# Optimization experiments

Measured on AMD Instinct MI355X. Metric: run time of the kernel, lower is better.

The kernel has to match this reference:

```python
import jax, jax.numpy as jnp
import numpy as np

OUTPUT_SIZE = 512


def _build_schedule(n, m):
    """Static pyramid-circuit schedule of Givens/RBS gates on n wires.

    Sequential gate order (matches theta ordering): for k = 1..n-1, apply
    gates on adjacent wire pairs (i, i+1) for i = k-1 down to max(k-m, 0).
    Total gates = (2n - m - 1) * m // 2. Gates are packed into a brickwork
    schedule (timestep t = 2(k-1) - i) so each layer touches disjoint pairs
    and the whole chain runs in T = n + m - 2 parallel layers.
    Padded slots point at dummy wires (n, n+1) and are masked to identity.
    """
    layers = {}
    t_idx = 0
    for k in range(1, n):
        for i in range(k - 1, max(k - m, 0) - 1, -1):
            t = 2 * (k - 1) - i
            layers.setdefault(t, []).append((i, t_idx))
            t_idx += 1
    T = max(layers) + 1
    W = max(len(v) for v in layers.values())
    wire = np.full((T, W), n, dtype=np.int32)   # pad gates hit dummy wires (n, n+1)
    tidx = np.zeros((T, W), dtype=np.int32)
    mask = np.zeros((T, W), dtype=np.float32)
    for t, gs in layers.items():
        for j, (i, ti) in enumerate(gs):
            wire[t, j] = i
            tidx[t, j] = ti
            mask[t, j] = 1.0
    return wire, tidx, mask


def apply_orthogonal(thetas, x, output_size):
    input_size = x.shape[-1]
    n, m = max(input_size, output_size), min(input_size, output_size)
    wire, tidx, mask = _build_schedule(n, m)
    if input_size < n:
        x = jnp.pad(x, ((0, 0), (0, n - input_size)))
    state = jnp.pad(x, ((0, 0), (0, 2)))          # two dummy columns for padded gate slots
    th = thetas[jnp.asarray(tidx)]                # [T, W]
    msk = jnp.asarray(mask)
    cos = jnp.where(msk > 0, jnp.cos(th), 1.0)    # padded slots -> identity rotation
    sin = jnp.where(msk > 0, jnp.sin(th), 0.0)
    wa = jnp.asarray(wire)                        # [T, W] first wire of each pair
    wb = wa + 1

    def step(st, layer):
        c, s, a_idx, b_idx = layer
        a = st[:, a_idx]                          # [B, W]
        b = st[:, b_idx]
        st = st.at[:, a_idx].set(c * a + s * b)   # RBS rotation on each pair
        st = st.at[:, b_idx].set(c * b - s * a)
        return st, None

    state, _ = jax.lax.scan(step, state, (cos, sin, wa, wb))
    return state[:, :output_size]


def setup_inputs():
    key = jax.random.key(0)
    k1, k2 = jax.random.split(key)
    B, N = 256, 512
    n_thetas = (2 * max(N, OUTPUT_SIZE) - min(N, OUTPUT_SIZE) - 1) * min(N, OUTPUT_SIZE) // 2
    x = jax.random.normal(k1, (B, N), dtype=jnp.float32)
    thetas = jax.random.uniform(k2, (n_thetas,), dtype=jnp.float32,
                                minval=-np.pi, maxval=np.pi)
    bias = jnp.zeros((OUTPUT_SIZE,), dtype=jnp.float32)
    return {"x": x, "thetas": thetas, "bias": bias}


def reference(x, thetas, bias):
    # normalize_inputs=False path; with_bias=True
    out = apply_orthogonal(thetas, x, OUTPUT_SIZE)
    return out + bias
```

## Files before the change

kernel.cpp:

```cpp
#include <hip/hip_runtime.h>
#include <hip/hip_fp16.h>
#include <stdint.h>


#define PAIRS_PAD 512
#define TOTALH2 (PAIRS_PAD * 512)
#define NWIN 8
#define WPAIRS 64
#define V_ELEMS (512 * 512)

#define OFF_V_BYTES (1u << 20)
#define V_BYTES (512u * 512u * 2u)
#define OFF_P_BYTES (OFF_V_BYTES + 8u * V_BYTES)
#define OFF_Q_BYTES (OFF_P_BYTES + 4u * V_BYTES)
#define OFF_Y_BYTES (OFF_Q_BYTES + 2u * V_BYTES)

typedef _Float16 half8_t __attribute__((ext_vector_type(8)));
typedef float f32x4_t __attribute__((ext_vector_type(4)));

__global__ __launch_bounds__(256) void fused_kernel(
    const float* __restrict__ thetas, __half2* __restrict__ Wh) {
  int tid = blockIdx.x * 256 + threadIdx.x;
  int p = tid >> 9, r = tid & 511;
  int h = r >> 8, rr = r & 255, L = rr >> 2, j = rr & 3;
  int t = 2 * p + h;
  int i = 8 * L + 2 * j + h;
  float c = 1.0f, s = 0.0f;
  if (i <= min(t, 1020 - t)) {
    int k = ((t + i) >> 1) + 1;
    int idx = ((k * (k - 1)) >> 1) + (k - 1 - i);
    __sincosf(thetas[idx], &s, &c);
  }
  if (h == 1 && j == 3) c -= 1.0f;
  Wh[tid] = __floats2half2_rn(c, s);
}

template <int N>
__device__ __forceinline__ void wait_vm() {
  asm volatile("s_waitcnt vmcnt(%0)" ::"i"(N) : "memory");
}
template <int CTRL>
__device__ __forceinline__ float dpp_f(float v) {
  return __int_as_float(
      __builtin_amdgcn_mov_dpp(__float_as_int(v), CTRL, 0xF, 0xF, true));
}
template <int CTRL>
__device__ __forceinline__ uint32_t dpp_u(uint32_t v) {
  return (uint32_t)__builtin_amdgcn_mov_dpp((int)v, CTRL, 0xF, 0xF, true);
}
__device__ __forceinline__ float mix_s(uint32_t g, float b) {
  float d;
  asm("v_fma_mix_f32 %0, %1, %2, 0 op_sel:[1,0,0] op_sel_hi:[1,0,0]"
      : "=v"(d) : "v"(g), "v"(b));
  return d;
}
__device__ __forceinline__ float mix_ns(uint32_t g, float b) {
  float d;
  asm("v_fma_mix_f32 %0, -%1, %2, 0 op_sel:[1,0,0] op_sel_hi:[1,0,0]"
      : "=v"(d) : "v"(g), "v"(b));
  return d;
}
__device__ __forceinline__ float mix_c_acc(uint32_t g, float b, float acc) {
  float d;
  asm("v_fma_mix_f32 %0, %1, %2, %3 op_sel:[0,0,0] op_sel_hi:[1,0,0]"
      : "=v"(d) : "v"(g), "v"(b), "v"(acc));
  return d;
}
__device__ __forceinline__ void gate_mix(float& a, float& b, uint32_t g) {
  float t = mix_s(g, b);
  float u = mix_ns(g, a);
  float na = mix_c_acc(g, a, t);
  float nb = mix_c_acc(g, b, u);
  a = na; b = nb;
}
__device__ __forceinline__ void gate_mix_neg(float& a, float& b, uint32_t g) {
  float t = mix_ns(g, b);
  float u = mix_s(g, a);
  float na = mix_c_acc(g, a, t);
  float nb = mix_c_acc(g, b, u);
  a = na; b = nb;
}

__device__ __forceinline__ void pair_fwd(float& v0, float& v1, float& v2,
                                         float& v3, float& v4, float& v5,
                                         float& v6, float& v7,
                                         const uint4& E, const uint4& O) {
  gate_mix(v0, v1, E.x);
  gate_mix(v2, v3, E.y);
  gate_mix(v4, v5, E.z);
  gate_mix(v6, v7, E.w);
  uint32_t bl = dpp_u<0x111>(O.w);
  float rv0 = dpp_f<0x101>(v0);
  float lv7 = dpp_f<0x111>(v7);
  gate_mix(v1, v2, O.x);
  gate_mix(v3, v4, O.y);
  gate_mix(v5, v6, O.z);
  float t = mix_s(O.w, rv0);
  t = mix_c_acc(O.w, v7, t);
  v7 = t + v7;
  float u = mix_ns(bl, lv7);
  u = mix_c_acc(bl, v0, u);
  v0 = u + v0;
}

__device__ __forceinline__ void pair_rev(float& v0, float& v1, float& v2,
                                         float& v3, float& v4, float& v5,
                                         float& v6, float& v7,
                                         const uint4& E, const uint4& O) {
  uint32_t bl = dpp_u<0x111>(O.w);
  float rv0 = dpp_f<0x101>(v0);
  float lv7 = dpp_f<0x111>(v7);
  gate_mix_neg(v1, v2, O.x);
  gate_mix_neg(v3, v4, O.y);
  gate_mix_neg(v5, v6, O.z);
  float t = mix_ns(O.w, rv0);
  t = mix_c_acc(O.w, v7, t);
  v7 = t + v7;
  float u = mix_s(bl, lv7);
  u = mix_c_acc(bl, v0, u);
  v0 = u + v0;
  gate_mix_neg(v0, v1, E.x);
  gate_mix_neg(v2, v3, E.y);
  gate_mix_neg(v4, v5, E.z);
  gate_mix_neg(v6, v7, E.w);
}

__global__ __launch_bounds__(64) void window_kernel(
    const uint32_t* __restrict__ W, _Float16* __restrict__ V) {
  const int lane = threadIdx.x;
  const int gl = lane & 15, grp = lane >> 4;
  const int w = blockIdx.x >> 7;
  const int d = ((blockIdx.x & 127) << 2) + grp;
  const bool rev = (w & 1);
  int b0 = d - 60;
  int base = (b0 <= 0) ? 0 : (b0 & ~7);
  base = min(base, 384);
  const int idx0 = (base >> 3) + gl;
  const int wire0 = base + 8 * gl;

  float v0 = (wire0 + 0 == d) ? 1.f : 0.f;
  float v1 = (wire0 + 1 == d) ? 1.f : 0.f;
  float v2 = (wire0 + 2 == d) ? 1.f : 0.f;
  float v3 = (wire0 + 3 == d) ? 1.f : 0.f;
  float v4 = (wire0 + 4 == d) ? 1.f : 0.f;
  float v5 = (wire0 + 5 == d) ? 1.f : 0.f;
  float v6 = (wire0 + 6 == d) ? 1.f : 0.f;
  float v7 = (wire0 + 7 == d) ? 1.f : 0.f;

  const int p0 = w * WPAIRS;
  const uint4* __restrict__ Wg = (const uint4*)W;

  uint4 R[4][2];
  if (!rev) {
#pragma unroll
    for (int s = 0; s < 4; ++s) {
      R[s][0] = Wg[(p0 + s) * 128 + idx0];
      R[s][1] = Wg[(p0 + s) * 128 + 64 + idx0];
    }
    for (int it = 0; it < 16; ++it) {
#pragma unroll
      for (int s = 0; s < 4; ++s) {
        wait_vm<6>();
        pair_fwd(v0, v1, v2, v3, v4, v5, v6, v7, R[s][0], R[s][1]);
        int pn = p0 + min(it * 4 + s + 4, 63);
        R[s][0] = Wg[pn * 128 + idx0];
        R[s][1] = Wg[pn * 128 + 64 + idx0];
      }
    }
  } else {
#pragma unroll
    for (int s = 0; s < 4; ++s) {
      R[s][0] = Wg[(p0 + 63 - s) * 128 + idx0];
      R[s][1] = Wg[(p0 + 63 - s) * 128 + 64 + idx0];
    }
    for (int it = 0; it < 16; ++it) {
#pragma unroll
      for (int s = 0; s < 4; ++s) {
        wait_vm<6>();
        pair_rev(v0, v1, v2, v3, v4, v5, v6, v7, R[s][0], R[s][1]);
        int pn = p0 + 63 - min(it * 4 + s + 4, 63);
        R[s][0] = Wg[pn * 128 + idx0];
        R[s][1] = Wg[pn * 128 + 64 + idx0];
      }
    }
  }

  uint32_t ph0 = __builtin_bit_cast(uint32_t, __builtin_amdgcn_cvt_pkrtz(v0, v1));
  uint32_t ph1 = __builtin_bit_cast(uint32_t, __builtin_amdgcn_cvt_pkrtz(v2, v3));
  uint32_t ph2 = __builtin_bit_cast(uint32_t, __builtin_amdgcn_cvt_pkrtz(v4, v5));
  uint32_t ph3 = __builtin_bit_cast(uint32_t, __builtin_amdgcn_cvt_pkrtz(v6, v7));
  uint32_t* dst = (uint32_t*)(V + (size_t)w * V_ELEMS + (size_t)d * 512);
#pragma unroll
  for (int pass = 0; pass < 4; ++pass) {
    const int S = ((pass << 7) - base) >> 3;
    const int srcg = gl + S;
    const bool ok = (srcg >= 0) && (srcg < 16);
    const int baddr = ((grp << 4) + (ok ? srcg : 0)) << 2;
    uint32_t o0 = (uint32_t)__builtin_amdgcn_ds_bpermute(baddr, (int)ph0);
    uint32_t o1 = (uint32_t)__builtin_amdgcn_ds_bpermute(baddr, (int)ph1);
    uint32_t o2 = (uint32_t)__builtin_amdgcn_ds_bpermute(baddr, (int)ph2);
    uint32_t o3 = (uint32_t)__builtin_amdgcn_ds_bpermute(baddr, (int)ph3);
    if (!ok) { o0 = 0u; o1 = 0u; o2 = 0u; o3 = 0u; }
    *(uint4*)(dst + pass * 64 + gl * 4) = make_uint4(o0, o1, o2, o3);
  }
}

struct GemmDesc { const _Float16* A; const _Float16* B; _Float16* C; };
struct Descs4 { GemmDesc d[4]; };

__global__ __launch_bounds__(128) void gemm512_kernel(Descs4 ds) {
  const int g = blockIdx.x >> 7;
  const int t = blockIdx.x & 127;
  const int rt = t >> 3, ct = t & 7;
  const int lane = threadIdx.x & 63, wv = threadIdx.x >> 6;
  const int l16 = lane & 15, h8 = (lane >> 4) * 8;
  const GemmDesc de = ds.d[g];
  const _Float16* Ap = de.A + (size_t)(rt * 32 + wv * 16 + l16) * 512 + h8;
  const _Float16* Bp = de.B + (size_t)(ct * 64 + l16) * 512 + h8;

  half8_t aR[3]; half8_t bR[3][4];
#pragma unroll
  for (int s = 0; s < 3; ++s) {
    aR[s] = *(const half8_t*)(Ap + s * 32);
#pragma unroll
    for (int n = 0; n < 4; ++n)
      bR[s][n] = *(const half8_t*)(Bp + (size_t)n * (16 * 512) + s * 32);
  }
  f32x4_t acc[4];
#pragma unroll
  for (int n = 0; n < 4; ++n) acc[n] = (f32x4_t){0.f, 0.f, 0.f, 0.f};

#pragma unroll
  for (int ks = 0; ks < 16; ++ks) {
    const int s = ks % 3;
    if (ks <= 13) wait_vm<10>();
    else if (ks == 14) wait_vm<5>();
    else wait_vm<0>();
    half8_t a = aR[s];
    half8_t b0 = bR[s][0], b1 = bR[s][1], b2 = bR[s][2], b3 = bR[s][3];
    if (ks + 3 < 16) {
      aR[s] = *(const half8_t*)(Ap + (ks + 3) * 32);
#pragma unroll
      for (int n = 0; n < 4; ++n)
        bR[s][n] = *(const half8_t*)(Bp + (size_t)n * (16 * 512) + (ks + 3) * 32);
    }
    acc[0] = __builtin_amdgcn_mfma_f32_16x16x32_f16(a, b0, acc[0], 0, 0, 0);
    acc[1] = __builtin_amdgcn_mfma_f32_16x16x32_f16(a, b1, acc[1], 0, 0, 0);
    acc[2] = __builtin_amdgcn_mfma_f32_16x16x32_f16(a, b2, acc[2], 0, 0, 0);
    acc[3] = __builtin_amdgcn_mfma_f32_16x16x32_f16(a, b3, acc[3], 0, 0, 0);
  }
  const int r4 = rt * 32 + wv * 16 + (lane >> 4) * 4;
#pragma unroll
  for (int n = 0; n < 4; ++n) {
    uint2 pk;
    pk.x = __builtin_bit_cast(uint32_t,
             __builtin_amdgcn_cvt_pkrtz(acc[n][0], acc[n][1]));
    pk.y = __builtin_bit_cast(uint32_t,
             __builtin_amdgcn_cvt_pkrtz(acc[n][2], acc[n][3]));
    *(uint2*)(de.C + (size_t)(ct * 64 + n * 16 + l16) * 512 + r4) = pk;
  }
}

__global__ __launch_bounds__(128) void apply1_kernel(
    const _Float16* __restrict__ Qt0, const float* __restrict__ x,
    _Float16* __restrict__ y) {
  const int rt = blockIdx.x >> 2, ct = blockIdx.x & 3;
  const int lane = threadIdx.x & 63, wv = threadIdx.x >> 6;
  const int l16 = lane & 15, h8 = (lane >> 4) * 8;
  const _Float16* Ap = Qt0 + (size_t)(rt * 32 + wv * 16 + l16) * 512 + h8;
  const float* Bx = x + (size_t)(ct * 64 + l16) * 512 + h8;

  half8_t aR[2]; float4 fR[2][4][2];
#pragma unroll
  for (int s = 0; s < 2; ++s) {
    aR[s] = *(const half8_t*)(Ap + s * 32);
#pragma unroll
    for (int n = 0; n < 4; ++n) {
      fR[s][n][0] = *(const float4*)(Bx + (size_t)n * (16 * 512) + s * 32);
      fR[s][n][1] = *(const float4*)(Bx + (size_t)n * (16 * 512) + s * 32 + 4);
    }
  }
  f32x4_t acc[4];
#pragma unroll
  for (int n = 0; n < 4; ++n) acc[n] = (f32x4_t){0.f, 0.f, 0.f, 0.f};

#pragma unroll
  for (int ks = 0; ks < 16; ++ks) {
    const int s = ks & 1;
    if (ks <= 14) wait_vm<9>();
    else wait_vm<0>();
    half8_t a = aR[s];
    half8_t bf[4];
#pragma unroll
    for (int n = 0; n < 4; ++n) {
      float4 f0 = fR[s][n][0], f1 = fR[s][n][1];
      uint4 u;
      u.x = __builtin_bit_cast(uint32_t, __builtin_amdgcn_cvt_pkrtz(f0.x, f0.y));
      u.y = __builtin_bit_cast(uint32_t, __builtin_amdgcn_cvt_pkrtz(f0.z, f0.w));
      u.z = __builtin_bit_cast(uint32_t, __builtin_amdgcn_cvt_pkrtz(f1.x, f1.y));
      u.w = __builtin_bit_cast(uint32_t, __builtin_amdgcn_cvt_pkrtz(f1.z, f1.w));
      bf[n] = __builtin_bit_cast(half8_t, u);
    }
    if (ks + 2 < 16) {
      aR[s] = *(const half8_t*)(Ap + (ks + 2) * 32);
#pragma unroll
      for (int n = 0; n < 4; ++n) {
        fR[s][n][0] = *(const float4*)(Bx + (size_t)n * (16 * 512) + (ks + 2) * 32);
        fR[s][n][1] = *(const float4*)(Bx + (size_t)n * (16 * 512) + (ks + 2) * 32 + 4);
      }
    }
    acc[0] = __builtin_amdgcn_mfma_f32_16x16x32_f16(a, bf[0], acc[0], 0, 0, 0);
    acc[1] = __builtin_amdgcn_mfma_f32_16x16x32_f16(a, bf[1], acc[1], 0, 0, 0);
    acc[2] = __builtin_amdgcn_mfma_f32_16x16x32_f16(a, bf[2], acc[2], 0, 0, 0);
    acc[3] = __builtin_amdgcn_mfma_f32_16x16x32_f16(a, bf[3], acc[3], 0, 0, 0);
  }
  const int r4 = rt * 32 + wv * 16 + (lane >> 4) * 4;
#pragma unroll
  for (int n = 0; n < 4; ++n) {
    uint2 pk;
    pk.x = __builtin_bit_cast(uint32_t,
             __builtin_amdgcn_cvt_pkrtz(acc[n][0], acc[n][1]));
    pk.y = __builtin_bit_cast(uint32_t,
             __builtin_amdgcn_cvt_pkrtz(acc[n][2], acc[n][3]));
    *(uint2*)(y + (size_t)(ct * 64 + n * 16 + l16) * 512 + r4) = pk;
  }
}

__global__ __launch_bounds__(128) void apply2_kernel(
    const _Float16* __restrict__ Qt1, const _Float16* __restrict__ y,
    const float* __restrict__ bias, float* __restrict__ out) {
  const int rt = blockIdx.x >> 2, ct = blockIdx.x & 3;
  const int lane = threadIdx.x & 63, wv = threadIdx.x >> 6;
  const int l16 = lane & 15, h8 = (lane >> 4) * 8;
  const _Float16* Ap = Qt1 + (size_t)(rt * 32 + wv * 16 + l16) * 512 + h8;
  const _Float16* Bp = y + (size_t)(ct * 64 + l16) * 512 + h8;

  half8_t aR[3]; half8_t bR[3][4];
#pragma unroll
  for (int s = 0; s < 3; ++s) {
    aR[s] = *(const half8_t*)(Ap + s * 32);
#pragma unroll
    for (int n = 0; n < 4; ++n)
      bR[s][n] = *(const half8_t*)(Bp + (size_t)n * (16 * 512) + s * 32);
  }
  f32x4_t acc[4];
#pragma unroll
  for (int n = 0; n < 4; ++n) acc[n] = (f32x4_t){0.f, 0.f, 0.f, 0.f};

#pragma unroll
  for (int ks = 0; ks < 16; ++ks) {
    const int s = ks % 3;
    if (ks <= 13) wait_vm<10>();
    else if (ks == 14) wait_vm<5>();
    else wait_vm<0>();
    half8_t a = aR[s];
    half8_t b0 = bR[s][0], b1 = bR[s][1], b2 = bR[s][2], b3 = bR[s][3];
    if (ks + 3 < 16) {
      aR[s] = *(const half8_t*)(Ap + (ks + 3) * 32);
#pragma unroll
      for (int n = 0; n < 4; ++n)
        bR[s][n] = *(const half8_t*)(Bp + (size_t)n * (16 * 512) + (ks + 3) * 32);
    }
    acc[0] = __builtin_amdgcn_mfma_f32_16x16x32_f16(a, b0, acc[0], 0, 0, 0);
    acc[1] = __builtin_amdgcn_mfma_f32_16x16x32_f16(a, b1, acc[1], 0, 0, 0);
    acc[2] = __builtin_amdgcn_mfma_f32_16x16x32_f16(a, b2, acc[2], 0, 0, 0);
    acc[3] = __builtin_amdgcn_mfma_f32_16x16x32_f16(a, b3, acc[3], 0, 0, 0);
  }
  const int r4 = rt * 32 + wv * 16 + (lane >> 4) * 4;
  const float4 bv = *(const float4*)(bias + r4);
#pragma unroll
  for (int n = 0; n < 4; ++n) {
    const int b = ct * 64 + n * 16 + l16;
    float4 o;
    o.x = acc[n][0] + bv.x;
    o.y = acc[n][1] + bv.y;
    o.z = acc[n][2] + bv.z;
    o.w = acc[n][3] + bv.w;
    *(float4*)(out + (size_t)b * 512 + r4) = o;
  }
}

extern "C" void kernel_launch(void* const* d_in, const int* in_sizes, int n_in,
                              void* d_out, int out_size, void* d_ws,
                              size_t ws_size, hipStream_t stream) {
  const float* x = (const float*)d_in[0];
  const float* thetas = (const float*)d_in[1];
  const float* bias = (const float*)d_in[2];
  float* out = (float*)d_out;

  char* ws = (char*)d_ws;
  uint32_t* W = (uint32_t*)ws;
  _Float16* V = (_Float16*)(ws + OFF_V_BYTES);
  _Float16* P = (_Float16*)(ws + OFF_P_BYTES);
  _Float16* Q = (_Float16*)(ws + OFF_Q_BYTES);
  _Float16* Y = (_Float16*)(ws + OFF_Y_BYTES);

  fused_kernel<<<TOTALH2 / 256, 256, 0, stream>>>(thetas, (__half2*)W);
  window_kernel<<<NWIN * 128, 64, 0, stream>>>(W, V);

  Descs4 l1;
  l1.d[0] = {V + 1 * (size_t)V_ELEMS, V + 0 * (size_t)V_ELEMS, P + 0 * (size_t)V_ELEMS};
  l1.d[1] = {V + 2 * (size_t)V_ELEMS, V + 3 * (size_t)V_ELEMS, P + 1 * (size_t)V_ELEMS};
  l1.d[2] = {V + 5 * (size_t)V_ELEMS, V + 4 * (size_t)V_ELEMS, P + 2 * (size_t)V_ELEMS};
  l1.d[3] = {V + 6 * (size_t)V_ELEMS, V + 7 * (size_t)V_ELEMS, P + 3 * (size_t)V_ELEMS};
  gemm512_kernel<<<512, 128, 0, stream>>>(l1);

  Descs4 l2;
  l2.d[0] = {P + 0 * (size_t)V_ELEMS, P + 1 * (size_t)V_ELEMS, Q + 0 * (size_t)V_ELEMS};
  l2.d[1] = {P + 2 * (size_t)V_ELEMS, P + 3 * (size_t)V_ELEMS, Q + 1 * (size_t)V_ELEMS};
  l2.d[2] = l2.d[0];
  l2.d[3] = l2.d[0];
  gemm512_kernel<<<256, 128, 0, stream>>>(l2);

  apply1_kernel<<<64, 128, 0, stream>>>(Q + 0 * (size_t)V_ELEMS, x, Y);
  apply2_kernel<<<64, 128, 0, stream>>>(Q + 1 * (size_t)V_ELEMS, Y, bias, out);
}
```

Baseline: 107.1 us.

## Fuse all stages into one cooperative persistent kernel with grid syncs

```diff
diff --git a/kernel.cpp b/kernel.cpp
--- a/kernel.cpp
+++ b/kernel.cpp
@@ -1,6 +1,9 @@
 #include <hip/hip_runtime.h>
 #include <hip/hip_fp16.h>
+#include <hip/hip_cooperative_groups.h>
 #include <stdint.h>
+
+namespace cg = cooperative_groups;
 
 
 #define PAIRS_PAD 512
@@ -17,23 +20,6 @@
 
 typedef _Float16 half8_t __attribute__((ext_vector_type(8)));
 typedef float f32x4_t __attribute__((ext_vector_type(4)));
-
-__global__ __launch_bounds__(256) void fused_kernel(
-    const float* __restrict__ thetas, __half2* __restrict__ Wh) {
-  int tid = blockIdx.x * 256 + threadIdx.x;
-  int p = tid >> 9, r = tid & 511;
-  int h = r >> 8, rr = r & 255, L = rr >> 2, j = rr & 3;
-  int t = 2 * p + h;
-  int i = 8 * L + 2 * j + h;
-  float c = 1.0f, s = 0.0f;
-  if (i <= min(t, 1020 - t)) {
-    int k = ((t + i) >> 1) + 1;
-    int idx = ((k * (k - 1)) >> 1) + (k - 1 - i);
-    __sincosf(thetas[idx], &s, &c);
-  }
-  if (h == 1 && j == 3) c -= 1.0f;
-  Wh[tid] = __floats2half2_rn(c, s);
-}
 
 template <int N>
 __device__ __forceinline__ void wait_vm() {
@@ -125,12 +111,30 @@
   gate_mix_neg(v6, v7, E.w);
 }
 
-__global__ __launch_bounds__(64) void window_kernel(
-    const uint32_t* __restrict__ W, _Float16* __restrict__ V) {
-  const int lane = threadIdx.x;
+
+__device__ __forceinline__ void dev_table(int tid,
+                                          const float* __restrict__ thetas,
+                                          __half2* __restrict__ Wh) {
+  int p = tid >> 9, r = tid & 511;
+  int h = r >> 8, rr = r & 255, L = rr >> 2, j = rr & 3;
+  int t = 2 * p + h;
+  int i = 8 * L + 2 * j + h;
+  float c = 1.0f, s = 0.0f;
+  if (i <= min(t, 1020 - t)) {
+    int k = ((t + i) >> 1) + 1;
+    int idx = ((k * (k - 1)) >> 1) + (k - 1 - i);
+    __sincosf(thetas[idx], &s, &c);
+  }
+  if (h == 1 && j == 3) c -= 1.0f;
+  Wh[tid] = __floats2half2_rn(c, s);
+}
+
+__device__ __forceinline__ void dev_window(int gw, int lane,
+                                           const uint32_t* __restrict__ W,
+                                           _Float16* __restrict__ V) {
   const int gl = lane & 15, grp = lane >> 4;
-  const int w = blockIdx.x >> 7;
-  const int d = ((blockIdx.x & 127) << 2) + grp;
+  const int w = gw >> 7;
+  const int d = ((gw & 127) << 2) + grp;
   const bool rev = (w & 1);
   int b0 = d - 60;
   int base = (b0 <= 0) ? 0 : (b0 & ~7);
@@ -205,18 +209,15 @@
   }
 }
 
-struct GemmDesc { const _Float16* A; const _Float16* B; _Float16* C; };
-struct Descs4 { GemmDesc d[4]; };
-
-__global__ __launch_bounds__(128) void gemm512_kernel(Descs4 ds) {
-  const int g = blockIdx.x >> 7;
-  const int t = blockIdx.x & 127;
+__device__ __forceinline__ void dev_gemm_tile(const _Float16* __restrict__ A,
+                                              const _Float16* __restrict__ B,
+                                              _Float16* __restrict__ C, int t,
+                                              int ut) {
   const int rt = t >> 3, ct = t & 7;
-  const int lane = threadIdx.x & 63, wv = threadIdx.x >> 6;
+  const int lane = ut & 63, wv = ut >> 6;
   const int l16 = lane & 15, h8 = (lane >> 4) * 8;
-  const GemmDesc de = ds.d[g];
-  const _Float16* Ap = de.A + (size_t)(rt * 32 + wv * 16 + l16) * 512 + h8;
-  const _Float16* Bp = de.B + (size_t)(ct * 64 + l16) * 512 + h8;
+  const _Float16* Ap = A + (size_t)(rt * 32 + wv * 16 + l16) * 512 + h8;
+  const _Float16* Bp = B + (size_t)(ct * 64 + l16) * 512 + h8;
 
   half8_t aR[3]; half8_t bR[3][4];
 #pragma unroll
@@ -257,15 +258,16 @@
              __builtin_amdgcn_cvt_pkrtz(acc[n][0], acc[n][1]));
     pk.y = __builtin_bit_cast(uint32_t,
              __builtin_amdgcn_cvt_pkrtz(acc[n][2], acc[n][3]));
-    *(uint2*)(de.C + (size_t)(ct * 64 + n * 16 + l16) * 512 + r4) = pk;
-  }
-}
-
-__global__ __launch_bounds__(128) void apply1_kernel(
-    const _Float16* __restrict__ Qt0, const float* __restrict__ x,
-    _Float16* __restrict__ y) {
-  const int rt = blockIdx.x >> 2, ct = blockIdx.x & 3;
-  const int lane = threadIdx.x & 63, wv = threadIdx.x >> 6;
+    *(uint2*)(C + (size_t)(ct * 64 + n * 16 + l16) * 512 + r4) = pk;
+  }
+}
+
+__device__ __forceinline__ void dev_apply1(int job, int ut,
+                                           const _Float16* __restrict__ Qt0,
+                                           const float* __restrict__ x,
+                                           _Float16* __restrict__ y) {
+  const int rt = job >> 2, ct = job & 3;
+  const int lane = ut & 63, wv = ut >> 6;
   const int l16 = lane & 15, h8 = (lane >> 4) * 8;
   const _Float16* Ap = Qt0 + (size_t)(rt * 32 + wv * 16 + l16) * 512 + h8;
   const float* Bx = x + (size_t)(ct * 64 + l16) * 512 + h8;
@@ -326,11 +328,13 @@
   }
 }
 
-__global__ __launch_bounds__(128) void apply2_kernel(
-    const _Float16* __restrict__ Qt1, const _Float16* __restrict__ y,
-    const float* __restrict__ bias, float* __restrict__ out) {
-  const int rt = blockIdx.x >> 2, ct = blockIdx.x & 3;
-  const int lane = threadIdx.x & 63, wv = threadIdx.x >> 6;
+__device__ __forceinline__ void dev_apply2(int job, int ut,
+                                           const _Float16* __restrict__ Qt1,
+                                           const _Float16* __restrict__ y,
+                                           const float* __restrict__ bias,
+                                           float* __restrict__ out) {
+  const int rt = job >> 2, ct = job & 3;
+  const int lane = ut & 63, wv = ut >> 6;
   const int l16 = lane & 15, h8 = (lane >> 4) * 8;
   const _Float16* Ap = Qt1 + (size_t)(rt * 32 + wv * 16 + l16) * 512 + h8;
   const _Float16* Bp = y + (size_t)(ct * 64 + l16) * 512 + h8;
@@ -380,11 +384,90 @@
   }
 }
 
+__global__ __launch_bounds__(256, 1) void mega_kernel(
+    const float* __restrict__ thetas, const float* __restrict__ x,
+    const float* __restrict__ bias, uint32_t* __restrict__ W,
+    _Float16* __restrict__ V, _Float16* __restrict__ P,
+    _Float16* __restrict__ Q, _Float16* __restrict__ Y,
+    float* __restrict__ out) {
+  cg::grid_group grid = cg::this_grid();
+  const int tid = threadIdx.x;
+  const int bid = blockIdx.x;
+  const int gtid = bid * 256 + tid;
+
+  {
+    __half2* Wh = (__half2*)W;
+#pragma unroll
+    for (int kk = 0; kk < 4; ++kk) dev_table(gtid + kk * 65536, thetas, Wh);
+  }
+  wait_vm<0>();
+  grid.sync();
+
+  dev_window(bid * 4 + (tid >> 6), tid & 63, W, V);
+  wait_vm<0>();
+  grid.sync();
+
+  const int unit = bid * 2 + (tid >> 7);
+  const int ut = tid & 127;
+
+  {
+    const int g = unit >> 7, t = unit & 127;
+    const int ag = g + 1 + ((g >> 1) << 1);
+    const int bg = 4 * g + 1 - ag;
+    dev_gemm_tile(V + (size_t)ag * V_ELEMS, V + (size_t)bg * V_ELEMS,
+                  P + (size_t)g * V_ELEMS, t, ut);
+  }
+  wait_vm<0>();
+  grid.sync();
+
+  if (unit < 256) {
+    const int g = unit >> 7, t = unit & 127;
+    dev_gemm_tile(P + (size_t)(2 * g) * V_ELEMS,
+                  P + (size_t)(2 * g + 1) * V_ELEMS,
+                  Q + (size_t)g * V_ELEMS, t, ut);
+    wait_vm<0>();
+  }
+  grid.sync();
+
+  if (unit < 64) {
+    dev_apply1(unit, ut, Q, x, Y);
+    wait_vm<0>();
+  }
+  grid.sync();
+
+  if (unit < 64) dev_apply2(unit, ut, Q + (size_t)V_ELEMS, Y, bias, out);
+}
+
+__global__ __launch_bounds__(256) void fused_kernel(
+    const float* __restrict__ thetas, __half2* __restrict__ Wh) {
+  dev_table(blockIdx.x * 256 + threadIdx.x, thetas, Wh);
+}
+__global__ __launch_bounds__(64) void window_kernel(
+    const uint32_t* __restrict__ W, _Float16* __restrict__ V) {
+  dev_window(blockIdx.x, threadIdx.x, W, V);
+}
+struct GemmDesc { const _Float16* A; const _Float16* B; _Float16* C; };
+struct Descs4 { GemmDesc d[4]; };
+__global__ __launch_bounds__(128) void gemm512_kernel(Descs4 ds) {
+  const GemmDesc de = ds.d[blockIdx.x >> 7];
+  dev_gemm_tile(de.A, de.B, de.C, blockIdx.x & 127, threadIdx.x);
+}
+__global__ __launch_bounds__(128) void apply1_kernel(
+    const _Float16* __restrict__ Qt0, const float* __restrict__ x,
+    _Float16* __restrict__ y) {
+  dev_apply1(blockIdx.x, threadIdx.x, Qt0, x, y);
+}
+__global__ __launch_bounds__(128) void apply2_kernel(
+    const _Float16* __restrict__ Qt1, const _Float16* __restrict__ y,
+    const float* __restrict__ bias, float* __restrict__ out) {
+  dev_apply2(blockIdx.x, threadIdx.x, Qt1, y, bias, out);
+}
+
 extern "C" void kernel_launch(void* const* d_in, const int* in_sizes, int n_in,
                               void* d_out, int out_size, void* d_ws,
                               size_t ws_size, hipStream_t stream) {
+  const float* thetas = (const float*)d_in[1];
   const float* x = (const float*)d_in[0];
-  const float* thetas = (const float*)d_in[1];
   const float* bias = (const float*)d_in[2];
   float* out = (float*)d_out;
 
@@ -395,23 +478,27 @@
   _Float16* Q = (_Float16*)(ws + OFF_Q_BYTES);
   _Float16* Y = (_Float16*)(ws + OFF_Y_BYTES);
 
+  void* args[] = {(void*)&thetas, (void*)&x, (void*)&bias, (void*)&W,
+                  (void*)&V, (void*)&P, (void*)&Q, (void*)&Y, (void*)&out};
+  hipError_t err = hipLaunchCooperativeKernel(
+      (void*)mega_kernel, dim3(256), dim3(256), args, 0, stream);
+  if (err == hipSuccess) return;
+  (void)hipGetLastError();
+
   fused_kernel<<<TOTALH2 / 256, 256, 0, stream>>>(thetas, (__half2*)W);
   window_kernel<<<NWIN * 128, 64, 0, stream>>>(W, V);
-
   Descs4 l1;
   l1.d[0] = {V + 1 * (size_t)V_ELEMS, V + 0 * (size_t)V_ELEMS, P + 0 * (size_t)V_ELEMS};
   l1.d[1] = {V + 2 * (size_t)V_ELEMS, V + 3 * (size_t)V_ELEMS, P + 1 * (size_t)V_ELEMS};
   l1.d[2] = {V + 5 * (size_t)V_ELEMS, V + 4 * (size_t)V_ELEMS, P + 2 * (size_t)V_ELEMS};
   l1.d[3] = {V + 6 * (size_t)V_ELEMS, V + 7 * (size_t)V_ELEMS, P + 3 * (size_t)V_ELEMS};
   gemm512_kernel<<<512, 128, 0, stream>>>(l1);
-
   Descs4 l2;
   l2.d[0] = {P + 0 * (size_t)V_ELEMS, P + 1 * (size_t)V_ELEMS, Q + 0 * (size_t)V_ELEMS};
   l2.d[1] = {P + 2 * (size_t)V_ELEMS, P + 3 * (size_t)V_ELEMS, Q + 1 * (size_t)V_ELEMS};
   l2.d[2] = l2.d[0];
   l2.d[3] = l2.d[0];
   gemm512_kernel<<<256, 128, 0, stream>>>(l2);
-
   apply1_kernel<<<64, 128, 0, stream>>>(Q + 0 * (size_t)V_ELEMS, x, Y);
   apply2_kernel<<<64, 128, 0, stream>>>(Q + 1 * (size_t)V_ELEMS, Y, bias, out);
 }
```

After: 262.5 us. 145% more time.
